# Kernel optimization log

Hardware: AMD Instinct MI355X
Metric: run time of the kernel (lower is better)

The kernel has to match this reference:

```python
import jax, jax.numpy as jnp
import numpy as np

HID = 2048
NH = 16
HD = HID // NH  # 128
THETA = 10000.0


def _rope_cos_sin(position_ids):
    # inv_freq: [HD/2]
    inv_freq = 1.0 / (THETA ** (jnp.arange(0, HD, 2, dtype=jnp.float32) / HD))
    freqs = position_ids.astype(jnp.float32)[:, :, None] * inv_freq[None, None, :]  # [b,s,hd/2]
    emb = jnp.concatenate([freqs, freqs], axis=-1)  # [b,s,hd]
    return jnp.cos(emb), jnp.sin(emb)


def _rotate_half(x):
    x1, x2 = x[..., : HD // 2], x[..., HD // 2:]
    return jnp.concatenate([-x2, x1], axis=-1)


def setup_inputs() -> dict:
    key = jax.random.key(0)
    ks = jax.random.split(key, 10)
    b, s = 2, 2048
    scale = 1.0 / np.sqrt(HID)
    hidden_states = jax.random.normal(ks[0], (b, s, HID), dtype=jnp.float32)
    wq = jax.random.normal(ks[1], (HID, HID), dtype=jnp.float32) * scale
    wk = jax.random.normal(ks[2], (HID, HID), dtype=jnp.float32) * scale
    wv = jax.random.normal(ks[3], (HID, HID), dtype=jnp.float32) * scale
    wo = jax.random.normal(ks[4], (HID, HID), dtype=jnp.float32) * scale
    bq = jnp.zeros((HID,), jnp.float32)
    bk = jnp.zeros((HID,), jnp.float32)
    bv = jnp.zeros((HID,), jnp.float32)
    bo = jnp.zeros((HID,), jnp.float32)
    # HF-style additive causal mask [b,1,q,kv]: 0 on/below diag, large negative above
    neg = jnp.finfo(jnp.float32).min
    causal = jnp.where(jnp.tril(jnp.ones((s, s), dtype=bool)), 0.0, neg)
    attention_mask = jnp.broadcast_to(causal[None, None], (b, 1, s, s)).astype(jnp.float32)
    position_ids = jnp.broadcast_to(jnp.arange(s, dtype=jnp.int32)[None], (b, s))
    return {
        "hidden_states": hidden_states,
        "wq": wq, "bq": bq, "wk": wk, "bk": bk,
        "wv": wv, "bv": bv, "wo": wo, "bo": bo,
        "attention_mask": attention_mask, "position_ids": position_ids,
    }


def reference(hidden_states, wq, bq, wk, bk, wv, bv, wo, bo, attention_mask, position_ids):
    b, s, _ = hidden_states.shape
    q = hidden_states @ wq.T + bq  # [b,s,hid]
    k = hidden_states @ wk.T + bk
    v = hidden_states @ wv.T + bv
    # [b, nh, s, hd]
    q = q.reshape(b, s, NH, HD).transpose(0, 2, 1, 3)
    k = k.reshape(b, s, NH, HD).transpose(0, 2, 1, 3)
    v = v.reshape(b, s, NH, HD).transpose(0, 2, 1, 3)
    cos, sin = _rope_cos_sin(position_ids)  # [b,s,hd]
    cos, sin = cos[:, None], sin[:, None]  # unsqueeze_dim=1 -> [b,1,s,hd]
    q = q * cos + _rotate_half(q) * sin
    k = k * cos + _rotate_half(k) * sin
    scores = jnp.einsum("bhqd,bhkd->bhqk", q, k) / np.sqrt(HD)
    scores = scores + attention_mask
    attn = jax.nn.softmax(scores.astype(jnp.float32), axis=-1).astype(q.dtype)
    out = jnp.einsum("bhqk,bhkd->bhqd", attn, v)  # [b,nh,s,hd]
    out = out.transpose(0, 2, 1, 3).reshape(b, s, HID)
    return out @ wo.T + bo
```

## Files before the change

### kernel.cpp

```cpp
#include <hip/hip_runtime.h>

#define S_LEN 2048
#define HID   2048
#define NHEAD 16
#define HDIM  128
#define BATCH 2
#define KDIM  2048

using bf16x8  = __attribute__((ext_vector_type(8))) short;
using f32x4   = __attribute__((ext_vector_type(4))) float;
using f32x16  = __attribute__((ext_vector_type(16))) float;
using short4v = __attribute__((ext_vector_type(4))) short;
using uint4v  = __attribute__((ext_vector_type(4))) unsigned;

__device__ __forceinline__ short f2bf(float f) {
  union { float f; unsigned u; } v; v.f = f;
  unsigned r = v.u + 0x7fffu + ((v.u >> 16) & 1u);
  return (short)(r >> 16);
}
__device__ __forceinline__ float bf2f(short s) {
  union { unsigned u; float f; } v;
  v.u = ((unsigned)(unsigned short)s) << 16;
  return v.f;
}

__device__ __forceinline__ void gl_lds16(const void* g, void* l) {
  __builtin_amdgcn_global_load_lds(
      (const __attribute__((address_space(1))) void*)g,
      (__attribute__((address_space(3))) void*)l, 16, 0, 0);
}

__global__ __launch_bounds__(256)
void convert_all(const float* __restrict__ hs, const float* __restrict__ wq,
                 const float* __restrict__ wk, const float* __restrict__ wv,
                 const float* __restrict__ wo,
                 short* __restrict__ hsb, short* __restrict__ wqkv,
                 short* __restrict__ wob)
{
  const int base = blockIdx.x * 256 + threadIdx.x;
#pragma unroll
  for (int it = 0; it < 6; ++it) {
    int j = base + it * 524288;
    const float* src; short* dst;
    if (j < 1048576)      { src = hs; dst = hsb; }
    else if (j < 1572864) { j -= 1048576; src = wq; dst = wqkv; }
    else if (j < 2097152) { j -= 1572864; src = wk; dst = wqkv + 4194304; }
    else if (j < 2621440) { j -= 2097152; src = wv; dst = wqkv + 8388608; }
    else                  { j -= 2621440; src = wo; dst = wob; }
    f32x4 a = ((const f32x4*)src)[2 * j];
    f32x4 b = ((const f32x4*)src)[2 * j + 1];
    bf16x8 o;
    o[0]=f2bf(a[0]); o[1]=f2bf(a[1]); o[2]=f2bf(a[2]); o[3]=f2bf(a[3]);
    o[4]=f2bf(b[0]); o[5]=f2bf(b[1]); o[6]=f2bf(b[2]); o[7]=f2bf(b[3]);
    ((bf16x8*)dst)[j] = o;
  }
}

template<int KIND>
__global__ __launch_bounds__(256)
void gemm128(const short* __restrict__ A, const short* __restrict__ B,
             const float* __restrict__ bias0, const float* __restrict__ bias1,
             const float* __restrict__ bias2,
             void* __restrict__ O0, void* __restrict__ O1, void* __restrict__ O2)
{
  __shared__ __align__(16) short As[128 * 64];
  __shared__ __align__(16) short Bs[128 * 64];
  const int tid  = threadIdx.x;
  const int lane = tid & 63, wave = tid >> 6;
  const int ln = lane & 15, g = lane >> 4;
  const int wr = wave >> 1, wc = wave & 1;
  const int m0 = blockIdx.x * 128, n0 = blockIdx.y * 128;

  const int srow   = tid >> 3;
  const int schunk = (tid & 7) ^ (srow & 7);
  const short* aS = A + (size_t)(m0 + srow) * KDIM + schunk * 8;
  const short* bS = B + (size_t)(n0 + srow) * KDIM + schunk * 8;

  f32x4 acc[4][4] = {};

  for (int k0 = 0; k0 < KDIM; k0 += 64) {
    __syncthreads();
#pragma unroll
    for (int j = 0; j < 4; ++j) {
      gl_lds16(aS + k0 + j * (32 * KDIM), &As[j * 2048 + tid * 8]);
      gl_lds16(bS + k0 + j * (32 * KDIM), &Bs[j * 2048 + tid * 8]);
    }
    __syncthreads();

#pragma unroll
    for (int ks = 0; ks < 2; ++ks) {
      bf16x8 af[4], bfm[4];
#pragma unroll
      for (int i = 0; i < 4; ++i) {
        const int r = wr * 64 + i * 16 + ln;
        af[i] = *(const bf16x8*)&As[r * 64 + (((ks * 4 + g) ^ (r & 7)) << 3)];
      }
#pragma unroll
      for (int j2 = 0; j2 < 4; ++j2) {
        const int r = wc * 64 + j2 * 16 + ln;
        bfm[j2] = *(const bf16x8*)&Bs[r * 64 + (((ks * 4 + g) ^ (r & 7)) << 3)];
      }
#pragma unroll
      for (int i = 0; i < 4; ++i)
#pragma unroll
        for (int j2 = 0; j2 < 4; ++j2)
          acc[i][j2] = __builtin_amdgcn_mfma_f32_16x16x32_bf16(af[i], bfm[j2], acc[i][j2], 0, 0, 0);
    }
  }

  if constexpr (KIND == 0) {
    const int seg   = n0 >> 11;
    const int nbase = (n0 & 2047) + wc * 64;
    const float* bias = (seg == 0) ? bias0 : (seg == 1) ? bias1 : bias2;
    float bvv[4];
#pragma unroll
    for (int j = 0; j < 4; ++j) bvv[j] = bias[nbase + j * 16 + ln];
    if (seg < 2) {
      short* C = (short*)(seg ? O1 : O0);
#pragma unroll
      for (int i = 0; i < 4; ++i) {
        const int mb = m0 + wr * 64 + i * 16 + 4 * g;
#pragma unroll
        for (int j = 0; j < 4; ++j) {
          const int nl = nbase + j * 16 + ln;
          const int h = nl >> 7, d = nl & 127;
#pragma unroll
          for (int e = 0; e < 4; ++e) {
            const int m = mb + e, bb = m >> 11, t = m & (S_LEN - 1);
            C[((size_t)((bb * NHEAD + h) * S_LEN + t) << 7) + d] = f2bf(acc[i][j][e] + bvv[j]);
          }
        }
      }
    } else {
      short* C = (short*)O2;
#pragma unroll
      for (int i = 0; i < 4; ++i) {
        const int mb = m0 + wr * 64 + i * 16 + 4 * g;
        const int bb = mb >> 11, t0 = mb & (S_LEN - 1);
#pragma unroll
        for (int j = 0; j < 4; ++j) {
          const int nl = nbase + j * 16 + ln;
          const int h = nl >> 7, d = nl & 127;
          short4v v;
#pragma unroll
          for (int e = 0; e < 4; ++e) v[e] = f2bf(acc[i][j][e] + bvv[j]);
          *(short4v*)&C[((size_t)((bb * NHEAD + h) * HDIM + d)) * S_LEN + t0] = v;
        }
      }
    }
  } else {
    float* C = (float*)O0;
    float bvv[4];
#pragma unroll
    for (int j = 0; j < 4; ++j) bvv[j] = bias0[n0 + wc * 64 + j * 16 + ln];
#pragma unroll
    for (int i = 0; i < 4; ++i) {
      const int mb = m0 + wr * 64 + i * 16 + 4 * g;
#pragma unroll
      for (int j = 0; j < 4; ++j) {
        const int n = n0 + wc * 64 + j * 16 + ln;
#pragma unroll
        for (int e = 0; e < 4; ++e)
          C[(size_t)(mb + e) * HID + n] = acc[i][j][e] + bvv[j];
      }
    }
  }
}

#define QSCALE 0.12752767502f
__global__ __launch_bounds__(256)
void rope_kernel(short* __restrict__ Qb, short* __restrict__ Kb,
                 const int* __restrict__ pos_ids)
{
  const int row = blockIdx.x * 4 + (threadIdx.x >> 6);
  const int d   = threadIdx.x & 63;
  const int bh  = row >> 11, t = row & (S_LEN - 1);
  const int b   = bh >> 4;
  const float pos = (float)pos_ids[b * S_LEN + t];
  const float inv = exp2f((float)d * -0.20762050593f);
  float s, c;
  sincosf(pos * inv, &s, &c);
  const size_t base = (size_t)row * HDIM;
  {
    float x1 = bf2f(Qb[base + d]), x2 = bf2f(Qb[base + d + 64]);
    Qb[base + d]      = f2bf((x1 * c - x2 * s) * QSCALE);
    Qb[base + d + 64] = f2bf((x2 * c + x1 * s) * QSCALE);
  }
  {
    float x1 = bf2f(Kb[base + d]), x2 = bf2f(Kb[base + d + 64]);
    Kb[base + d]      = f2bf(x1 * c - x2 * s);
    Kb[base + d + 64] = f2bf(x2 * c + x1 * s);
  }
}

__global__ __launch_bounds__(256, 2)
void attn_kernel(const short* __restrict__ Qb, const short* __restrict__ Kb,
                 const short* __restrict__ Vt, short* __restrict__ AO)
{
  __shared__ __align__(16) short Ks[128 * 128];
  __shared__ __align__(16) short Vs[128 * 128];
  const int tid  = threadIdx.x;
  const int wave = tid >> 6, lane = tid & 63;
  const int lq = lane & 31, lh = lane >> 5;
  const int bid = blockIdx.x;
  const int bh  = bid & 31;
  const int grp = bid >> 5;
  const int yt  = (grp & 7) ^ ((grp & 8) ? 15 : 0);
  const int qw  = yt * 128 + wave * 32;
  const int q   = qw + lq;

  const short* Kbh = Kb + (size_t)bh * (S_LEN * HDIM);
  const short* Vbh = Vt + (size_t)bh * (S_LEN * HDIM);
  const int sw   = ((tid & 15) ^ ((tid >> 4) & 7)) << 3;
  const int kOff = (tid >> 4) * HDIM + sw;
  const int vOff = (tid >> 4) * S_LEN + sw;

  bf16x8 qf[8];
#pragma unroll
  for (int kk = 0; kk < 8; ++kk)
    qf[kk] = *(const bf16x8*)&Qb[((size_t)bh * S_LEN + q) * HDIM + kk * 16 + lh * 8];

  f32x16 o[4] = {};
  float m_s = -3.0e38f, l_s = 0.f;

  for (int kvt = 0; kvt <= yt; ++kvt) {
    const int kv0 = kvt * 128;
    __syncthreads();
#pragma unroll
    for (int p = 0; p < 8; ++p) {
      gl_lds16(Kbh + (size_t)kv0 * HDIM + kOff + p * (16 * HDIM), &Ks[p * 2048 + tid * 8]);
      gl_lds16(Vbh + kv0 + vOff + p * (16 * S_LEN),               &Vs[p * 2048 + tid * 8]);
    }
    __syncthreads();

#pragma unroll
    for (int h = 0; h < 2; ++h) {
      f32x16 sfr[2] = {};
      __builtin_amdgcn_s_setprio(1);
#pragma unroll
      for (int kk = 0; kk < 8; ++kk) {
#pragma unroll
        for (int nt = 0; nt < 2; ++nt) {
          const int row = h * 64 + nt * 32 + lq;
          bf16x8 ak = *(const bf16x8*)&Ks[(row * 128 + kk * 16 + lh * 8) ^ ((row & 7) << 3)];
          sfr[nt] = __builtin_amdgcn_mfma_f32_32x32x16_bf16(ak, qf[kk], sfr[nt], 0, 0, 0);
        }
      }
      __builtin_amdgcn_s_setprio(0);

      if (kvt == yt) {
#pragma unroll
        for (int nt = 0; nt < 2; ++nt) {
          const int kvb = kv0 + h * 64 + nt * 32 + 4 * lh;
#pragma unroll
          for (int r = 0; r < 16; ++r) {
            const int kv = kvb + (r & 3) + 8 * (r >> 2);
            if (kv > q) sfr[nt][r] = -3.0e38f;
          }
        }
      }
      float rmax = -3.0e38f;
#pragma unroll
      for (int nt = 0; nt < 2; ++nt)
#pragma unroll
        for (int r = 0; r < 16; ++r) rmax = fmaxf(rmax, sfr[nt][r]);
      rmax = fmaxf(rmax, __shfl_xor(rmax, 32));

      if (__any(rmax > m_s + 8.0f)) {
        const float nm = fmaxf(m_s, rmax);
        const float corr = exp2f(m_s - nm);
        m_s = nm;
        l_s *= corr;
#pragma unroll
        for (int dt = 0; dt < 4; ++dt)
#pragma unroll
          for (int r = 0; r < 16; ++r) o[dt][r] *= corr;
      }

      float ps = 0.f;
#pragma unroll
      for (int nt = 0; nt < 2; ++nt)
#pragma unroll
        for (int r = 0; r < 16; ++r) {
          const float pv = exp2f(sfr[nt][r] - m_s);
          sfr[nt][r] = pv;
          ps += pv;
        }
      l_s += ps;

      bf16x8 pa[4];
#pragma unroll
      for (int kk = 0; kk < 4; ++kk) {
        const int nt = kk >> 1, c8 = (kk & 1) * 8;
        unsigned w0, w1, w2, w3;
        asm("v_cvt_pk_bf16_f32 %0, %1, %2" : "=v"(w0) : "v"(sfr[nt][c8 + 0]), "v"(sfr[nt][c8 + 1]));
        asm("v_cvt_pk_bf16_f32 %0, %1, %2" : "=v"(w1) : "v"(sfr[nt][c8 + 2]), "v"(sfr[nt][c8 + 3]));
        asm("v_cvt_pk_bf16_f32 %0, %1, %2" : "=v"(w2) : "v"(sfr[nt][c8 + 4]), "v"(sfr[nt][c8 + 5]));
        asm("v_cvt_pk_bf16_f32 %0, %1, %2" : "=v"(w3) : "v"(sfr[nt][c8 + 6]), "v"(sfr[nt][c8 + 7]));
        asm volatile("v_permlane32_swap_b32 %0, %1" : "+v"(w0), "+v"(w2));
        asm volatile("v_permlane32_swap_b32 %0, %1" : "+v"(w1), "+v"(w3));
        uint4v u; u[0] = w0; u[1] = w1; u[2] = w2; u[3] = w3;
        pa[kk] = __builtin_bit_cast(bf16x8, u);
      }

      __builtin_amdgcn_s_setprio(1);
#pragma unroll
      for (int kk = 0; kk < 4; ++kk) {
#pragma unroll
        for (int dt = 0; dt < 4; ++dt) {
          const int row = dt * 32 + lq;
          bf16x8 av = *(const bf16x8*)&Vs[(row * 128 + h * 64 + kk * 16 + lh * 8) ^ ((row & 7) << 3)];
          o[dt] = __builtin_amdgcn_mfma_f32_32x32x16_bf16(av, pa[kk], o[dt], 0, 0, 0);
        }
      }
      __builtin_amdgcn_s_setprio(0);
    }
  }

  l_s += __shfl_xor(l_s, 32);
  const float inv = 1.0f / l_s;
  const int b = bh >> 4, hh = bh & 15;
  short* dst = &AO[((size_t)b * S_LEN + q) * HID + hh * HDIM];
#pragma unroll
  for (int dt = 0; dt < 4; ++dt) {
#pragma unroll
    for (int rq = 0; rq < 4; ++rq) {
      short4v v4;
#pragma unroll
      for (int e = 0; e < 4; ++e) v4[e] = f2bf(o[dt][rq * 4 + e] * inv);
      *(short4v*)&dst[dt * 32 + rq * 8 + 4 * lh] = v4;
    }
  }
}

extern "C" void kernel_launch(void* const* d_in, const int* in_sizes, int n_in,
                              void* d_out, int out_size, void* d_ws, size_t ws_size,
                              hipStream_t stream)
{
  const float* hs = (const float*)d_in[0];
  const float* wq = (const float*)d_in[1];
  const float* bq = (const float*)d_in[2];
  const float* wk = (const float*)d_in[3];
  const float* bk = (const float*)d_in[4];
  const float* wv = (const float*)d_in[5];
  const float* bv = (const float*)d_in[6];
  const float* wo = (const float*)d_in[7];
  const float* bo = (const float*)d_in[8];
  const int*  pos = (const int*)d_in[10];
  float* out = (float*)d_out;

  const size_t TSZ = (size_t)BATCH * NHEAD * S_LEN * HDIM;
  short* Qb   = (short*)d_ws;
  short* Kb   = Qb + TSZ;
  short* Vt   = Kb + TSZ;
  short* hsb  = Vt + TSZ;
  short* AO   = hsb;
  short* Wqkv = hsb + TSZ;
  short* wob  = Wqkv + 12582912;

  convert_all<<<2048, 256, 0, stream>>>(hs, wq, wk, wv, wo, hsb, Wqkv, wob);
  gemm128<0><<<dim3(32, 48), 256, 0, stream>>>(hsb, Wqkv, bq, bk, bv, Qb, Kb, Vt);
  rope_kernel<<<(BATCH * NHEAD * S_LEN) / 4, 256, 0, stream>>>(Qb, Kb, pos);
  attn_kernel<<<512, 256, 0, stream>>>(Qb, Kb, Vt, AO);
  gemm128<1><<<dim3(32, 16), 256, 0, stream>>>(AO, wob, bo, nullptr, nullptr, out, nullptr, nullptr);
}
```

Before: 250.1 us.

## Double-buffer K/V tiles in attention kernel with 64-wide KV steps

Splits each 128-key KV tile into two 64-key stages held in double-buffered LDS and prefetches the next stage with async global-to-LDS loads while the current one is computed. A partial vmcnt wait plus barriers replace the old load-then-sync pattern. This aims to hide global load latency behind the MFMA and softmax work. The cost is more barriers and loop iterations, and the V tile layout and swizzle are rewritten, which risks bank conflicts or ordering bugs.

```diff
diff --git a/kernel.cpp b/kernel.cpp
--- a/kernel.cpp
+++ b/kernel.cpp
@@ -197,8 +197,8 @@
 void attn_kernel(const short* __restrict__ Qb, const short* __restrict__ Kb,
                  const short* __restrict__ Vt, short* __restrict__ AO)
 {
-  __shared__ __align__(16) short Ks[128 * 128];
-  __shared__ __align__(16) short Vs[128 * 128];
+  __shared__ __align__(16) short Ks[2][64 * 128];
+  __shared__ __align__(16) short Vs[2][128 * 64];
   const int tid  = threadIdx.x;
   const int wave = tid >> 6, lane = tid & 63;
   const int lq = lane & 31, lh = lane >> 5;
@@ -211,9 +211,8 @@
 
   const short* Kbh = Kb + (size_t)bh * (S_LEN * HDIM);
   const short* Vbh = Vt + (size_t)bh * (S_LEN * HDIM);
-  const int sw   = ((tid & 15) ^ ((tid >> 4) & 7)) << 3;
-  const int kOff = (tid >> 4) * HDIM + sw;
-  const int vOff = (tid >> 4) * S_LEN + sw;
+  const int kOff = (tid >> 4) * HDIM  + (((tid & 15) ^ ((tid >> 4) & 7)) << 3);
+  const int vOff = (tid >> 3) * S_LEN + (((tid & 7) ^ ((tid >> 3) & 7)) << 3);
 
   bf16x8 qf[8];
 #pragma unroll
@@ -223,98 +222,117 @@
   f32x16 o[4] = {};
   float m_s = -3.0e38f, l_s = 0.f;
 
-  for (int kvt = 0; kvt <= yt; ++kvt) {
-    const int kv0 = kvt * 128;
-    __syncthreads();
-#pragma unroll
-    for (int p = 0; p < 8; ++p) {
-      gl_lds16(Kbh + (size_t)kv0 * HDIM + kOff + p * (16 * HDIM), &Ks[p * 2048 + tid * 8]);
-      gl_lds16(Vbh + kv0 + vOff + p * (16 * S_LEN),               &Vs[p * 2048 + tid * 8]);
-    }
-    __syncthreads();
-
-#pragma unroll
-    for (int h = 0; h < 2; ++h) {
-      f32x16 sfr[2] = {};
-      __builtin_amdgcn_s_setprio(1);
-#pragma unroll
-      for (int kk = 0; kk < 8; ++kk) {
-#pragma unroll
-        for (int nt = 0; nt < 2; ++nt) {
-          const int row = h * 64 + nt * 32 + lq;
-          bf16x8 ak = *(const bf16x8*)&Ks[(row * 128 + kk * 16 + lh * 8) ^ ((row & 7) << 3)];
-          sfr[nt] = __builtin_amdgcn_mfma_f32_32x32x16_bf16(ak, qf[kk], sfr[nt], 0, 0, 0);
+  auto stage = [&](int kvt, int b) {
+    const int kv0 = kvt * 64;
+    const short* ks = Kbh + (size_t)kv0 * HDIM + kOff;
+    const short* vs = Vbh + kv0 + vOff;
+#pragma unroll
+    for (int j = 0; j < 4; ++j)
+      gl_lds16(ks + j * (16 * HDIM), &Ks[b][j * 2048 + tid * 8]);
+#pragma unroll
+    for (int j = 0; j < 4; ++j)
+      gl_lds16(vs + j * (32 * S_LEN), &Vs[b][j * 2048 + tid * 8]);
+  };
+
+  const int kvt_max = 2 * yt + 1;
+  stage(0, 0);
+  for (int kvt = 0; kvt <= kvt_max; ++kvt) {
+    const int cur = kvt & 1;
+    const int kv0 = kvt * 64;
+    if (kvt < kvt_max) {
+      stage(kvt + 1, cur ^ 1);
+      asm volatile("s_waitcnt vmcnt(8)" ::: "memory");
+    } else {
+      asm volatile("s_waitcnt vmcnt(0)" ::: "memory");
+    }
+    __builtin_amdgcn_s_barrier();
+    __builtin_amdgcn_sched_barrier(0);
+    const short* kb = &Ks[cur][0];
+    const short* vb = &Vs[cur][0];
+
+    f32x16 sfr[2] = {};
+    __builtin_amdgcn_s_setprio(1);
+#pragma unroll
+    for (int kk = 0; kk < 8; ++kk) {
+#pragma unroll
+      for (int nt = 0; nt < 2; ++nt) {
+        const int row = nt * 32 + lq;
+        bf16x8 ak = *(const bf16x8*)&kb[(row * 128 + kk * 16 + lh * 8) ^ ((row & 7) << 3)];
+        sfr[nt] = __builtin_amdgcn_mfma_f32_32x32x16_bf16(ak, qf[kk], sfr[nt], 0, 0, 0);
+      }
+    }
+    __builtin_amdgcn_s_setprio(0);
+
+    if (kvt >= 2 * yt) {
+#pragma unroll
+      for (int nt = 0; nt < 2; ++nt) {
+        const int kvb = kv0 + nt * 32 + 4 * lh;
+#pragma unroll
+        for (int r = 0; r < 16; ++r) {
+          const int kv = kvb + (r & 3) + 8 * (r >> 2);
+          if (kv > q) sfr[nt][r] = -3.0e38f;
         }
       }
-      __builtin_amdgcn_s_setprio(0);
-
-      if (kvt == yt) {
-#pragma unroll
-        for (int nt = 0; nt < 2; ++nt) {
-          const int kvb = kv0 + h * 64 + nt * 32 + 4 * lh;
-#pragma unroll
-          for (int r = 0; r < 16; ++r) {
-            const int kv = kvb + (r & 3) + 8 * (r >> 2);
-            if (kv > q) sfr[nt][r] = -3.0e38f;
-          }
-        }
-      }
-      float rmax = -3.0e38f;
-#pragma unroll
-      for (int nt = 0; nt < 2; ++nt)
-#pragma unroll
-        for (int r = 0; r < 16; ++r) rmax = fmaxf(rmax, sfr[nt][r]);
-      rmax = fmaxf(rmax, __shfl_xor(rmax, 32));
-
-      if (__any(rmax > m_s + 8.0f)) {
-        const float nm = fmaxf(m_s, rmax);
-        const float corr = exp2f(m_s - nm);
-        m_s = nm;
-        l_s *= corr;
-#pragma unroll
-        for (int dt = 0; dt < 4; ++dt)
-#pragma unroll
-          for (int r = 0; r < 16; ++r) o[dt][r] *= corr;
-      }
-
-      float ps = 0.f;
-#pragma unroll
-      for (int nt = 0; nt < 2; ++nt)
-#pragma unroll
-        for (int r = 0; r < 16; ++r) {
-          const float pv = exp2f(sfr[nt][r] - m_s);
-          sfr[nt][r] = pv;
-          ps += pv;
-        }
-      l_s += ps;
-
-      bf16x8 pa[4];
-#pragma unroll
-      for (int kk = 0; kk < 4; ++kk) {
-        const int nt = kk >> 1, c8 = (kk & 1) * 8;
-        unsigned w0, w1, w2, w3;
-        asm("v_cvt_pk_bf16_f32 %0, %1, %2" : "=v"(w0) : "v"(sfr[nt][c8 + 0]), "v"(sfr[nt][c8 + 1]));
-        asm("v_cvt_pk_bf16_f32 %0, %1, %2" : "=v"(w1) : "v"(sfr[nt][c8 + 2]), "v"(sfr[nt][c8 + 3]));
-        asm("v_cvt_pk_bf16_f32 %0, %1, %2" : "=v"(w2) : "v"(sfr[nt][c8 + 4]), "v"(sfr[nt][c8 + 5]));
-        asm("v_cvt_pk_bf16_f32 %0, %1, %2" : "=v"(w3) : "v"(sfr[nt][c8 + 6]), "v"(sfr[nt][c8 + 7]));
-        asm volatile("v_permlane32_swap_b32 %0, %1" : "+v"(w0), "+v"(w2));
-        asm volatile("v_permlane32_swap_b32 %0, %1" : "+v"(w1), "+v"(w3));
-        uint4v u; u[0] = w0; u[1] = w1; u[2] = w2; u[3] = w3;
-        pa[kk] = __builtin_bit_cast(bf16x8, u);
-      }
-
-      __builtin_amdgcn_s_setprio(1);
-#pragma unroll
-      for (int kk = 0; kk < 4; ++kk) {
-#pragma unroll
-        for (int dt = 0; dt < 4; ++dt) {
-          const int row = dt * 32 + lq;
-          bf16x8 av = *(const bf16x8*)&Vs[(row * 128 + h * 64 + kk * 16 + lh * 8) ^ ((row & 7) << 3)];
-          o[dt] = __builtin_amdgcn_mfma_f32_32x32x16_bf16(av, pa[kk], o[dt], 0, 0, 0);
-        }
-      }
-      __builtin_amdgcn_s_setprio(0);
-    }
+    }
+
+    float rmax = -3.0e38f;
+#pragma unroll
+    for (int nt = 0; nt < 2; ++nt)
+#pragma unroll
+      for (int r = 0; r < 16; ++r) rmax = fmaxf(rmax, sfr[nt][r]);
+    rmax = fmaxf(rmax, __shfl_xor(rmax, 32));
+
+    if (__any(rmax > m_s + 8.0f)) {
+      const float nm = fmaxf(m_s, rmax);
+      const float corr = exp2f(m_s - nm);
+      m_s = nm;
+      l_s *= corr;
+#pragma unroll
+      for (int dt = 0; dt < 4; ++dt)
+#pragma unroll
+        for (int r = 0; r < 16; ++r) o[dt][r] *= corr;
+    }
+
+    float ps = 0.f;
+#pragma unroll
+    for (int nt = 0; nt < 2; ++nt)
+#pragma unroll
+      for (int r = 0; r < 16; ++r) {
+        const float pv = exp2f(sfr[nt][r] - m_s);
+        sfr[nt][r] = pv;
+        ps += pv;
+      }
+    l_s += ps;
+
+    bf16x8 pa[4];
+#pragma unroll
+    for (int kk = 0; kk < 4; ++kk) {
+      const int nt = kk >> 1, c8 = (kk & 1) * 8;
+      unsigned w0, w1, w2, w3;
+      asm("v_cvt_pk_bf16_f32 %0, %1, %2" : "=v"(w0) : "v"(sfr[nt][c8 + 0]), "v"(sfr[nt][c8 + 1]));
+      asm("v_cvt_pk_bf16_f32 %0, %1, %2" : "=v"(w1) : "v"(sfr[nt][c8 + 2]), "v"(sfr[nt][c8 + 3]));
+      asm("v_cvt_pk_bf16_f32 %0, %1, %2" : "=v"(w2) : "v"(sfr[nt][c8 + 4]), "v"(sfr[nt][c8 + 5]));
+      asm("v_cvt_pk_bf16_f32 %0, %1, %2" : "=v"(w3) : "v"(sfr[nt][c8 + 6]), "v"(sfr[nt][c8 + 7]));
+      asm volatile("v_permlane32_swap_b32 %0, %1" : "+v"(w0), "+v"(w2));
+      asm volatile("v_permlane32_swap_b32 %0, %1" : "+v"(w1), "+v"(w3));
+      uint4v u; u[0] = w0; u[1] = w1; u[2] = w2; u[3] = w3;
+      pa[kk] = __builtin_bit_cast(bf16x8, u);
+    }
+
+    __builtin_amdgcn_s_setprio(1);
+#pragma unroll
+    for (int kk = 0; kk < 4; ++kk) {
+#pragma unroll
+      for (int dt = 0; dt < 4; ++dt) {
+        const int row = dt * 32 + lq;
+        bf16x8 av = *(const bf16x8*)&vb[(row * 64 + kk * 16 + lh * 8) ^ ((row & 7) << 3)];
+        o[dt] = __builtin_amdgcn_mfma_f32_32x32x16_bf16(av, pa[kk], o[dt], 0, 0, 0);
+      }
+    }
+    __builtin_amdgcn_s_setprio(0);
+
+    __builtin_amdgcn_sched_barrier(0);
+    __builtin_amdgcn_s_barrier();
   }
 
   l_s += __shfl_xor(l_s, 32);
```

Result: no change. 250.8 us (+0.3%).
